# Performance work log

Hardware: AMD Instinct MI355X
Metric: run time of the kernel (lower is better)

Reference implementation:

```python
import jax, jax.numpy as jnp
import numpy as np

L, D, FF, H, S, B = 6, 512, 2048, 8, 1024, 4
DH = D // H
EPS = 1e-5


def setup_inputs() -> dict:
    key = jax.random.key(0)
    ks = jax.random.split(key, 8)
    sd = 1.0 / np.sqrt(D)
    sf = 1.0 / np.sqrt(FF)
    return {
        'src': jax.random.normal(ks[0], (S, B, D), jnp.float32),
        'pos': jax.random.normal(ks[1], (S, B, D), jnp.float32) * 0.02,
        'Wq': jax.random.normal(ks[2], (L, D, D), jnp.float32) * sd,
        'bq': jnp.zeros((L, D), jnp.float32),
        'Wk': jax.random.normal(ks[3], (L, D, D), jnp.float32) * sd,
        'bk': jnp.zeros((L, D), jnp.float32),
        'Wv': jax.random.normal(ks[4], (L, D, D), jnp.float32) * sd,
        'bv': jnp.zeros((L, D), jnp.float32),
        'W1': jax.random.normal(ks[5], (L, D, FF), jnp.float32) * sd,
        'b1': jnp.zeros((L, FF), jnp.float32),
        'W2': jax.random.normal(ks[6], (L, FF, D), jnp.float32) * sf,
        'b2': jnp.zeros((L, D), jnp.float32),
        'ln1_g': jnp.ones((L, D), jnp.float32),
        'ln1_b': jnp.zeros((L, D), jnp.float32),
        'ln2_g': jnp.ones((L, D), jnp.float32),
        'ln2_b': jnp.zeros((L, D), jnp.float32),
        'lnf_g': jnp.ones((D,), jnp.float32),
        'lnf_b': jnp.zeros((D,), jnp.float32),
    }


def _layernorm(x, g, b):
    m = jnp.mean(x, axis=-1, keepdims=True)
    v = jnp.mean(jnp.square(x - m), axis=-1, keepdims=True)
    return (x - m) * jax.lax.rsqrt(v + EPS) * g + b


def _encoder(src, pos, Wq, bq, Wk, bk, Wv, bv, W1, b1, W2, b2,
             ln1_g, ln1_b, ln2_g, ln2_b, lnf_g, lnf_b):
    # src, pos: (S, B, D). Each layer internally transposes to (B, S, D) and the
    # encoder transposes back; equivalently work in (B, S, D) throughout the loop.
    x = (src + pos).transpose(1, 0, 2)  # (B, S, D)
    scale = 1.0 / np.sqrt(DH)
    for i in range(L):
        # --- self-attention block (pre-norm) ---
        x1 = _layernorm(x, ln1_g[i], ln1_b[i])
        q = (x1 @ Wq[i] + bq[i]).reshape(B, S, H, DH)
        k = (x1 @ Wk[i] + bk[i]).reshape(B, S, H, DH)
        v = (x1 @ Wv[i] + bv[i]).reshape(B, S, H, DH)
        scores = jnp.einsum('bqhd,bkhd->bhqk', q, k) * scale  # (B, H, S, S)
        probs = jax.nn.softmax(scores, axis=-1)
        ctx = jnp.einsum('bhqk,bkhd->bqhd', probs, v).reshape(B, S, D)
        x = x + ctx  # dropout=0.0 -> identity
        # --- feed-forward block (pre-norm) ---
        x2 = _layernorm(x, ln2_g[i], ln2_b[i])
        h = jax.nn.relu(x2 @ W1[i] + b1[i])
        x = x + (h @ W2[i] + b2[i])
    out = x.transpose(1, 0, 2)  # back to (S, B, D)
    return _layernorm(out, lnf_g, lnf_b)


def reference(src, pos, Wq, bq, Wk, bk, Wv, bv, W1, b1, W2, b2,
              ln1_g, ln1_b, ln2_g, ln2_b, lnf_g, lnf_b):
    return _encoder(src, pos, Wq, bq, Wk, bk, Wv, bv, W1, b1, W2, b2,
                    ln1_g, ln1_b, ln2_g, ln2_b, lnf_g, lnf_b)
```

## Files before the change

### kernel.cpp

```cpp
#include <hip/hip_runtime.h>

#define L_LAYERS 6
#define DMODEL 512
#define FFDIM 2048
#define NHEAD 8
#define SEQ 1024
#define BATCH 4
#define DHEAD 64
#define MROWS (BATCH*SEQ)

typedef __attribute__((ext_vector_type(4))) float f32x4;
typedef __attribute__((ext_vector_type(8))) unsigned short u16x8;
typedef __attribute__((ext_vector_type(8))) __bf16 bf16x8;

#define DEV static __device__ __forceinline__

DEV unsigned short f32_to_bf16(float f) {
  unsigned int u = __float_as_uint(f);
  u += 0x7fffu + ((u >> 16) & 1u);
  return (unsigned short)(u >> 16);
}
DEV float bf16_to_f32(unsigned short h) {
  return __uint_as_float(((unsigned int)h) << 16);
}
DEV f32x4 mfma_bf16(u16x8 a, u16x8 b, f32x4 c) {
  return __builtin_amdgcn_mfma_f32_16x16x32_bf16(
      __builtin_bit_cast(bf16x8, a), __builtin_bit_cast(bf16x8, b), c, 0, 0, 0);
}
DEV void gload16(const unsigned short* g, unsigned short* l) {
  __builtin_amdgcn_global_load_lds(
      (const __attribute__((address_space(1))) unsigned int*)g,
      (__attribute__((address_space(3))) unsigned int*)l, 16, 0, 0);
}

__global__ __launch_bounds__(256) void k_transpose(const float* __restrict__ Win,
                                                   unsigned short* __restrict__ Wout,
                                                   int K, int N) {
  __shared__ float t[32][33];
  Win  += (size_t)blockIdx.z * K * N;
  Wout += (size_t)blockIdx.z * K * N;
  int n0 = blockIdx.x * 32, k0 = blockIdx.y * 32;
  int lx = threadIdx.x & 31, ly = threadIdx.x >> 5;
  #pragma unroll
  for (int r = 0; r < 32; r += 8)
    t[ly + r][lx] = Win[(size_t)(k0 + ly + r) * N + n0 + lx];
  __syncthreads();
  #pragma unroll
  for (int r = 0; r < 32; r += 8)
    Wout[(size_t)(n0 + ly + r) * K + k0 + lx] = f32_to_bf16(t[lx][ly + r]);
}

__global__ __launch_bounds__(256) void k_addpos_ln(const float* __restrict__ src,
                                                   const float* __restrict__ pos,
                                                   const float* __restrict__ g,
                                                   const float* __restrict__ be,
                                                   float* __restrict__ x,
                                                   unsigned short* __restrict__ o) {
  int lane = threadIdx.x & 63, wv = threadIdx.x >> 6;
  int row = blockIdx.x * 4 + wv;
  int b = row >> 10, ss = row & (SEQ-1);
  const float* sr = src + (size_t)(ss*BATCH + b) * DMODEL + lane * 8;
  const float* pr = pos + (size_t)(ss*BATCH + b) * DMODEL + lane * 8;
  f32x4 v0 = *(const f32x4*)sr + *(const f32x4*)pr;
  f32x4 v1 = *(const f32x4*)(sr + 4) + *(const f32x4*)(pr + 4);
  float* xr = x + (size_t)row * DMODEL + lane * 8;
  *(f32x4*)xr = v0;
  *(f32x4*)(xr + 4) = v1;
  float s  = v0.x+v0.y+v0.z+v0.w + v1.x+v1.y+v1.z+v1.w;
  float s2 = v0.x*v0.x+v0.y*v0.y+v0.z*v0.z+v0.w*v0.w
           + v1.x*v1.x+v1.y*v1.y+v1.z*v1.z+v1.w*v1.w;
  #pragma unroll
  for (int off = 1; off < 64; off <<= 1) { s += __shfl_xor(s, off); s2 += __shfl_xor(s2, off); }
  float mean = s * (1.0f/DMODEL);
  float var  = s2 * (1.0f/DMODEL) - mean*mean;
  float rs = rsqrtf(var + 1e-5f);
  const float* gp = g + lane*8; const float* bp = be + lane*8;
  f32x4 g0 = *(const f32x4*)gp, g1 = *(const f32x4*)(gp+4);
  f32x4 b0 = *(const f32x4*)bp, b1v = *(const f32x4*)(bp+4);
  u16x8 r;
  r[0] = f32_to_bf16((v0.x-mean)*rs*g0.x + b0.x);
  r[1] = f32_to_bf16((v0.y-mean)*rs*g0.y + b0.y);
  r[2] = f32_to_bf16((v0.z-mean)*rs*g0.z + b0.z);
  r[3] = f32_to_bf16((v0.w-mean)*rs*g0.w + b0.w);
  r[4] = f32_to_bf16((v1.x-mean)*rs*g1.x + b1v.x);
  r[5] = f32_to_bf16((v1.y-mean)*rs*g1.y + b1v.y);
  r[6] = f32_to_bf16((v1.z-mean)*rs*g1.z + b1v.z);
  r[7] = f32_to_bf16((v1.w-mean)*rs*g1.w + b1v.w);
  *(u16x8*)(o + (size_t)row * DMODEL + lane * 8) = r;
}

__global__ __launch_bounds__(256) void k_ln_bf16(const float* __restrict__ x,
                                                 const float* __restrict__ g,
                                                 const float* __restrict__ be,
                                                 unsigned short* __restrict__ o) {
  int lane = threadIdx.x & 63, wv = threadIdx.x >> 6;
  int row = blockIdx.x * 4 + wv;
  const float* xr = x + (size_t)row * DMODEL + lane * 8;
  f32x4 v0 = *(const f32x4*)xr, v1 = *(const f32x4*)(xr + 4);
  float s  = v0.x+v0.y+v0.z+v0.w + v1.x+v1.y+v1.z+v1.w;
  float s2 = v0.x*v0.x+v0.y*v0.y+v0.z*v0.z+v0.w*v0.w
           + v1.x*v1.x+v1.y*v1.y+v1.z*v1.z+v1.w*v1.w;
  #pragma unroll
  for (int off = 1; off < 64; off <<= 1) { s += __shfl_xor(s, off); s2 += __shfl_xor(s2, off); }
  float mean = s * (1.0f/DMODEL);
  float var  = s2 * (1.0f/DMODEL) - mean*mean;
  float rs = rsqrtf(var + 1e-5f);
  const float* gp = g + lane*8; const float* bp = be + lane*8;
  f32x4 g0 = *(const f32x4*)gp, g1 = *(const f32x4*)(gp+4);
  f32x4 b0 = *(const f32x4*)bp, b1v = *(const f32x4*)(bp+4);
  u16x8 r;
  r[0] = f32_to_bf16((v0.x-mean)*rs*g0.x + b0.x);
  r[1] = f32_to_bf16((v0.y-mean)*rs*g0.y + b0.y);
  r[2] = f32_to_bf16((v0.z-mean)*rs*g0.z + b0.z);
  r[3] = f32_to_bf16((v0.w-mean)*rs*g0.w + b0.w);
  r[4] = f32_to_bf16((v1.x-mean)*rs*g1.x + b1v.x);
  r[5] = f32_to_bf16((v1.y-mean)*rs*g1.y + b1v.y);
  r[6] = f32_to_bf16((v1.z-mean)*rs*g1.z + b1v.z);
  r[7] = f32_to_bf16((v1.w-mean)*rs*g1.w + b1v.w);
  *(u16x8*)(o + (size_t)row * DMODEL + lane * 8) = r;
}

__global__ __launch_bounds__(256) void k_ln_final(const float* __restrict__ x,
                                                  const float* __restrict__ g,
                                                  const float* __restrict__ be,
                                                  float* __restrict__ out) {
  int lane = threadIdx.x & 63, wv = threadIdx.x >> 6;
  int row = blockIdx.x * 4 + wv;
  const float* xr = x + (size_t)row * DMODEL + lane * 8;
  f32x4 v0 = *(const f32x4*)xr, v1 = *(const f32x4*)(xr + 4);
  float s  = v0.x+v0.y+v0.z+v0.w + v1.x+v1.y+v1.z+v1.w;
  float s2 = v0.x*v0.x+v0.y*v0.y+v0.z*v0.z+v0.w*v0.w
           + v1.x*v1.x+v1.y*v1.y+v1.z*v1.z+v1.w*v1.w;
  #pragma unroll
  for (int off = 1; off < 64; off <<= 1) { s += __shfl_xor(s, off); s2 += __shfl_xor(s2, off); }
  float mean = s * (1.0f/DMODEL);
  float var  = s2 * (1.0f/DMODEL) - mean*mean;
  float rs = rsqrtf(var + 1e-5f);
  const float* gp = g + lane*8; const float* bp = be + lane*8;
  f32x4 g0 = *(const f32x4*)gp, g1 = *(const f32x4*)(gp+4);
  f32x4 b0 = *(const f32x4*)bp, b1v = *(const f32x4*)(bp+4);
  int b = row >> 10, ss = row & (SEQ-1);
  float* orow = out + (size_t)(ss*BATCH + b) * DMODEL + lane * 8;
  f32x4 o0, o1;
  o0.x = (v0.x-mean)*rs*g0.x + b0.x;  o0.y = (v0.y-mean)*rs*g0.y + b0.y;
  o0.z = (v0.z-mean)*rs*g0.z + b0.z;  o0.w = (v0.w-mean)*rs*g0.w + b0.w;
  o1.x = (v1.x-mean)*rs*g1.x + b1v.x; o1.y = (v1.y-mean)*rs*g1.y + b1v.y;
  o1.z = (v1.z-mean)*rs*g1.z + b1v.z; o1.w = (v1.w-mean)*rs*g1.w + b1v.w;
  *(f32x4*)orow = o0;
  *(f32x4*)(orow + 4) = o1;
}

#define BM 128
#define BN 128
#define BKK 32
#define NSL 4

DEV void gemm_core(const unsigned short* __restrict__ A,
                   const unsigned short* __restrict__ Bt,
                   int K, int m0, int n0,
                   unsigned short* As, unsigned short* Bs, f32x4 acc[4][4]) {
  const int tid = threadIdx.x;
  const int lane = tid & 63;
  const int w = tid >> 6;
  const int wr = w >> 1, wc = w & 1;
  const int l15 = lane & 15;
  const int ko = (lane >> 4) * 8;
  const int rl = lane >> 2;
  const int cc = (lane & 3) * 8;
  for (int kb = 0; kb < K; kb += NSL * BKK) {
    #pragma unroll
    for (int sl = 0; sl < NSL; ++sl) {
      #pragma unroll
      for (int i = 0; i < 2; ++i) {
        int r0 = w * 32 + i * 16;
        gload16(A  + (size_t)(m0 + r0 + rl) * K + kb + sl * BKK + cc, As + sl * (BM*BKK) + r0 * BKK);
        gload16(Bt + (size_t)(n0 + r0 + rl) * K + kb + sl * BKK + cc, Bs + sl * (BN*BKK) + r0 * BKK);
      }
    }
    __syncthreads();
    #pragma unroll
    for (int sl = 0; sl < NSL; ++sl) {
      const unsigned short* Asl = As + sl * (BM*BKK);
      const unsigned short* Bsl = Bs + sl * (BN*BKK);
      u16x8 af[4], bfr[4];
      #pragma unroll
      for (int m = 0; m < 4; ++m) af[m]  = *(const u16x8*)(Asl + (wr*64 + m*16 + l15) * BKK + ko);
      #pragma unroll
      for (int n = 0; n < 4; ++n) bfr[n] = *(const u16x8*)(Bsl + (wc*64 + n*16 + l15) * BKK + ko);
      #pragma unroll
      for (int m = 0; m < 4; ++m)
        #pragma unroll
        for (int n = 0; n < 4; ++n)
          acc[m][n] = mfma_bf16(af[m], bfr[n], acc[m][n]);
    }
    __syncthreads();
  }
}

__global__ __launch_bounds__(256) void k_gemm_qkv(
    const unsigned short* __restrict__ x1,
    const unsigned short* __restrict__ WqT, const unsigned short* __restrict__ WkT,
    const unsigned short* __restrict__ WvT,
    const float* __restrict__ bq, const float* __restrict__ bk, const float* __restrict__ bv,
    unsigned short* __restrict__ qo, unsigned short* __restrict__ ko2,
    unsigned short* __restrict__ vo) {
  __shared__ __align__(16) unsigned short As[NSL*BM*BKK];
  __shared__ __align__(16) unsigned short Bs[NSL*64*BKK];
  const int tid = threadIdx.x;
  const int lane = tid & 63;
  const int w = tid >> 6;
  const int wr = w >> 1, wc = w & 1;
  const int l15 = lane & 15;
  const int ko = (lane >> 4) * 8;
  const int rl = lane >> 2;
  const int cc = (lane & 3) * 8;
  const int m0 = blockIdx.x * BM;
  const int mat = blockIdx.y >> 3;
  const int n0 = (blockIdx.y & 7) * 64;
  const unsigned short* Bt = (mat == 0) ? WqT : ((mat == 1) ? WkT : WvT);
  const float* bias        = (mat == 0) ? bq  : ((mat == 1) ? bk  : bv);
  unsigned short* out      = (mat == 0) ? qo  : ((mat == 1) ? ko2 : vo);
  const float osc = (mat == 0) ? 0.125f : 1.0f;
  f32x4 acc[4][2];
  #pragma unroll
  for (int m = 0; m < 4; ++m)
    #pragma unroll
    for (int n = 0; n < 2; ++n) acc[m][n] = 0.0f;
  for (int kb = 0; kb < DMODEL; kb += NSL * BKK) {
    #pragma unroll
    for (int sl = 0; sl < NSL; ++sl) {
      #pragma unroll
      for (int i = 0; i < 2; ++i) {
        int r0 = w * 32 + i * 16;
        gload16(x1 + (size_t)(m0 + r0 + rl) * DMODEL + kb + sl * BKK + cc, As + sl * (BM*BKK) + r0 * BKK);
      }
      {
        int r0 = w * 16;
        gload16(Bt + (size_t)(n0 + r0 + rl) * DMODEL + kb + sl * BKK + cc, Bs + sl * (64*BKK) + r0 * BKK);
      }
    }
    __syncthreads();
    #pragma unroll
    for (int sl = 0; sl < NSL; ++sl) {
      const unsigned short* Asl = As + sl * (BM*BKK);
      const unsigned short* Bsl = Bs + sl * (64*BKK);
      u16x8 af[4], bfr[2];
      #pragma unroll
      for (int m = 0; m < 4; ++m) af[m]  = *(const u16x8*)(Asl + (wr*64 + m*16 + l15) * BKK + ko);
      #pragma unroll
      for (int n = 0; n < 2; ++n) bfr[n] = *(const u16x8*)(Bsl + (wc*32 + n*16 + l15) * BKK + ko);
      #pragma unroll
      for (int m = 0; m < 4; ++m)
        #pragma unroll
        for (int n = 0; n < 2; ++n)
          acc[m][n] = mfma_bf16(af[m], bfr[n], acc[m][n]);
    }
    __syncthreads();
  }
  const int g = lane >> 4;
  #pragma unroll
  for (int m = 0; m < 4; ++m) {
    #pragma unroll
    for (int n = 0; n < 2; ++n) {
      int col = n0 + wc*32 + n*16 + l15;
      int hh = col >> 6, dh = col & 63;
      float bval = bias[col];
      #pragma unroll
      for (int i = 0; i < 4; ++i) {
        int row = m0 + wr*64 + m*16 + g*4 + i;
        int bb = row >> 10, ss = row & (SEQ-1);
        size_t oidx;
        if (mat == 2)
          oidx = ((((size_t)(bb*NHEAD + hh)) * DHEAD + dh) << 10) + ss;
        else
          oidx = ((((size_t)(bb*NHEAD + hh)) << 10) + ss) * DHEAD + dh;
        out[oidx] = f32_to_bf16((acc[m][n][i] + bval) * osc);
      }
    }
  }
}

__global__ __launch_bounds__(256) void k_gemm_ffn1(
    const unsigned short* __restrict__ x1, const unsigned short* __restrict__ W1T,
    const float* __restrict__ b1, unsigned short* __restrict__ h) {
  __shared__ __align__(16) unsigned short As[NSL*BM*BKK];
  __shared__ __align__(16) unsigned short Bs[NSL*BN*BKK];
  int m0 = blockIdx.x * BM, n0 = blockIdx.y * BN;
  f32x4 acc[4][4];
  #pragma unroll
  for (int m = 0; m < 4; ++m)
    #pragma unroll
    for (int n = 0; n < 4; ++n) acc[m][n] = 0.0f;
  gemm_core(x1, W1T, DMODEL, m0, n0, As, Bs, acc);
  const int lane = threadIdx.x & 63;
  const int w = threadIdx.x >> 6; const int wr = w >> 1, wc = w & 1;
  #pragma unroll
  for (int m = 0; m < 4; ++m) {
    #pragma unroll
    for (int n = 0; n < 4; ++n) {
      int col = n0 + wc*64 + n*16 + (lane & 15);
      float bval = b1[col];
      #pragma unroll
      for (int i = 0; i < 4; ++i) {
        int row = m0 + wr*64 + m*16 + (lane >> 4)*4 + i;
        h[(size_t)row * FFDIM + col] = f32_to_bf16(fmaxf(acc[m][n][i] + bval, 0.0f));
      }
    }
  }
}

#define NSL2 8
__global__ __launch_bounds__(256) void k_gemm_ffn2(
    const unsigned short* __restrict__ h, const unsigned short* __restrict__ W2T,
    const float* __restrict__ b2, float* __restrict__ x) {
  __shared__ __align__(16) unsigned short As[NSL2*64*BKK];
  __shared__ __align__(16) unsigned short Bs[NSL2*64*BKK];
  const int tid = threadIdx.x;
  const int lane = tid & 63;
  const int w = tid >> 6;
  const int wr = w >> 1, wc = w & 1;
  const int l15 = lane & 15;
  const int ko = (lane >> 4) * 8;
  const int rl = lane >> 2;
  const int cc = (lane & 3) * 8;
  const int m0 = blockIdx.x * 64, n0 = blockIdx.y * 64;
  f32x4 acc[2][2];
  #pragma unroll
  for (int m = 0; m < 2; ++m)
    #pragma unroll
    for (int n = 0; n < 2; ++n) acc[m][n] = 0.0f;
  for (int kb = 0; kb < FFDIM; kb += NSL2 * BKK) {
    #pragma unroll
    for (int sl = 0; sl < NSL2; ++sl) {
      int r0 = w * 16;
      gload16(h   + (size_t)(m0 + r0 + rl) * FFDIM + kb + sl * BKK + cc, As + sl * (64*BKK) + r0 * BKK);
      gload16(W2T + (size_t)(n0 + r0 + rl) * FFDIM + kb + sl * BKK + cc, Bs + sl * (64*BKK) + r0 * BKK);
    }
    __syncthreads();
    #pragma unroll
    for (int sl = 0; sl < NSL2; ++sl) {
      const unsigned short* Asl = As + sl * (64*BKK);
      const unsigned short* Bsl = Bs + sl * (64*BKK);
      u16x8 af[2], bfr[2];
      #pragma unroll
      for (int m = 0; m < 2; ++m) af[m]  = *(const u16x8*)(Asl + (wr*32 + m*16 + l15) * BKK + ko);
      #pragma unroll
      for (int n = 0; n < 2; ++n) bfr[n] = *(const u16x8*)(Bsl + (wc*32 + n*16 + l15) * BKK + ko);
      #pragma unroll
      for (int m = 0; m < 2; ++m)
        #pragma unroll
        for (int n = 0; n < 2; ++n)
          acc[m][n] = mfma_bf16(af[m], bfr[n], acc[m][n]);
    }
    __syncthreads();
  }
  const int g = lane >> 4;
  #pragma unroll
  for (int m = 0; m < 2; ++m) {
    #pragma unroll
    for (int n = 0; n < 2; ++n) {
      int col = n0 + wc*32 + n*16 + l15;
      float bval = b2[col];
      #pragma unroll
      for (int i = 0; i < 4; ++i) {
        int row = m0 + wr*32 + m*16 + g*4 + i;
        size_t idx = (size_t)row * DMODEL + col;
        x[idx] = x[idx] + acc[m][n][i] + bval;
      }
    }
  }
}

#define KVBLK 128
#define KP 72
#define VP 136
#define NT (SEQ/KVBLK)

__global__ __launch_bounds__(512) void k_attn_mfma(
    const unsigned short* __restrict__ qb,
    const unsigned short* __restrict__ kb,
    const unsigned short* __restrict__ vtb,
    float* __restrict__ x) {
  __shared__ __align__(16) unsigned short Kl[2][KVBLK*KP];
  __shared__ __align__(16) unsigned short Vl[2][DHEAD*VP];
  __shared__ __align__(16) unsigned short Pl[8*16*VP];
  const int tid = threadIdx.x;
  const int w = tid >> 6, lane = tid & 63;
  const int c = lane & 15, g = lane >> 4;
  const int bh = blockIdx.x, qt = blockIdx.y;
  const int qw = qt * 128 + w * 16;
  const int krow = tid >> 2, kcol = (tid & 3) * 16;
  const int vrow = tid >> 3, vcol = (tid & 7) * 16;

  const unsigned short* kbase = kb + (size_t)bh * SEQ * DHEAD;
  const unsigned short* vbase = vtb + (size_t)bh * DHEAD * SEQ;

  u16x8 qf[2];
  {
    const unsigned short* qrow = qb + ((size_t)bh * SEQ + qw + c) * DHEAD;
    qf[0] = *(const u16x8*)(qrow + g * 8);
    qf[1] = *(const u16x8*)(qrow + 32 + g * 8);
  }
  f32x4 aco[4];
  #pragma unroll
  for (int n = 0; n < 4; ++n) aco[n] = 0.0f;
  float l_r = 0.0f;

  u16x8 kr0, kr1, vr0, vr1;
  kr0 = *(const u16x8*)(kbase + (size_t)krow * DHEAD + kcol);
  kr1 = *(const u16x8*)(kbase + (size_t)krow * DHEAD + kcol + 8);
  vr0 = *(const u16x8*)(vbase + (size_t)vrow * SEQ + vcol);
  vr1 = *(const u16x8*)(vbase + (size_t)vrow * SEQ + vcol + 8);
  *(u16x8*)(Kl[0] + krow * KP + kcol)     = kr0;
  *(u16x8*)(Kl[0] + krow * KP + kcol + 8) = kr1;
  *(u16x8*)(Vl[0] + vrow * VP + vcol)     = vr0;
  *(u16x8*)(Vl[0] + vrow * VP + vcol + 8) = vr1;
  __syncthreads();

  int cur = 0;
  for (int t = 0; t < NT; ++t) {
    if (t < NT - 1) {
      int kn = (t + 1) * KVBLK;
      kr0 = *(const u16x8*)(kbase + (size_t)(kn + krow) * DHEAD + kcol);
      kr1 = *(const u16x8*)(kbase + (size_t)(kn + krow) * DHEAD + kcol + 8);
      vr0 = *(const u16x8*)(vbase + (size_t)vrow * SEQ + kn + vcol);
      vr1 = *(const u16x8*)(vbase + (size_t)vrow * SEQ + kn + vcol + 8);
    }
    const unsigned short* Kt = Kl[cur];
    const unsigned short* Vt = Vl[cur];

    f32x4 s[8];
    #pragma unroll
    for (int n = 0; n < 8; ++n) s[n] = 0.0f;
    #pragma unroll
    for (int n = 0; n < 8; ++n) {
      #pragma unroll
      for (int kk = 0; kk < 2; ++kk) {
        u16x8 kf = *(const u16x8*)(Kt + (n * 16 + c) * KP + kk * 32 + g * 8);
        s[n] = mfma_bf16(kf, qf[kk], s[n]);
      }
    }

    float ps = 0.0f;
    {
      unsigned short* prow = Pl + (w * 16 + c) * VP;
      #pragma unroll
      for (int n = 0; n < 8; ++n) {
        float p0 = __expf(s[n][0]), p1 = __expf(s[n][1]);
        float p2 = __expf(s[n][2]), p3 = __expf(s[n][3]);
        ps += (p0 + p1) + (p2 + p3);
        *(unsigned int*)(prow + n * 16 + g * 4) =
            (unsigned)f32_to_bf16(p0) | ((unsigned)f32_to_bf16(p1) << 16);
        *(unsigned int*)(prow + n * 16 + g * 4 + 2) =
            (unsigned)f32_to_bf16(p2) | ((unsigned)f32_to_bf16(p3) << 16);
      }
    }
    ps += __shfl_xor(ps, 16);
    ps += __shfl_xor(ps, 32);
    l_r += ps;

    u16x8 pa[4];
    #pragma unroll
    for (int kk = 0; kk < 4; ++kk)
      pa[kk] = *(const u16x8*)(Pl + (w * 16 + c) * VP + kk * 32 + g * 8);
    #pragma unroll
    for (int n = 0; n < 4; ++n) {
      #pragma unroll
      for (int kk = 0; kk < 4; ++kk) {
        u16x8 vf = *(const u16x8*)(Vt + (n * 16 + c) * VP + kk * 32 + g * 8);
        aco[n] = mfma_bf16(pa[kk], vf, aco[n]);
      }
    }

    if (t < NT - 1) {
      unsigned short* Kn = Kl[cur ^ 1];
      unsigned short* Vn = Vl[cur ^ 1];
      *(u16x8*)(Kn + krow * KP + kcol)     = kr0;
      *(u16x8*)(Kn + krow * KP + kcol + 8) = kr1;
      *(u16x8*)(Vn + vrow * VP + vcol)     = vr0;
      *(u16x8*)(Vn + vrow * VP + vcol + 8) = vr1;
      __syncthreads();
    }
    cur ^= 1;
  }

  const int b = bh >> 3, h = bh & 7;
  #pragma unroll
  for (int i = 0; i < 4; ++i) {
    float lq = __shfl(l_r, g * 4 + i);
    float inv = 1.0f / lq;
    int q = qw + g * 4 + i;
    float* xr = x + ((size_t)b * SEQ + q) * DMODEL + h * DHEAD;
    #pragma unroll
    for (int n = 0; n < 4; ++n)
      xr[n * 16 + c] += aco[n][i] * inv;
  }
}

extern "C" void kernel_launch(void* const* d_in, const int* in_sizes, int n_in,
                              void* d_out, int out_size, void* d_ws, size_t ws_size,
                              hipStream_t stream) {
  const float* src  = (const float*)d_in[0];
  const float* pos  = (const float*)d_in[1];
  const float* Wq   = (const float*)d_in[2];
  const float* bq   = (const float*)d_in[3];
  const float* Wk   = (const float*)d_in[4];
  const float* bk   = (const float*)d_in[5];
  const float* Wv   = (const float*)d_in[6];
  const float* bv   = (const float*)d_in[7];
  const float* W1   = (const float*)d_in[8];
  const float* b1   = (const float*)d_in[9];
  const float* W2   = (const float*)d_in[10];
  const float* b2   = (const float*)d_in[11];
  const float* ln1g = (const float*)d_in[12];
  const float* ln1b = (const float*)d_in[13];
  const float* ln2g = (const float*)d_in[14];
  const float* ln2b = (const float*)d_in[15];
  const float* lnfg = (const float*)d_in[16];
  const float* lnfb = (const float*)d_in[17];

  char* p = (char*)d_ws;
  float* x = (float*)p;                      p += (size_t)MROWS * DMODEL * 4;
  unsigned short* x1 = (unsigned short*)p;   p += (size_t)MROWS * DMODEL * 2;
  unsigned short* qb = (unsigned short*)p;   p += (size_t)MROWS * DMODEL * 2;
  unsigned short* kbuf = (unsigned short*)p; p += (size_t)MROWS * DMODEL * 2;
  unsigned short* vtbuf = (unsigned short*)p; p += (size_t)MROWS * DMODEL * 2;
  unsigned short* hbuf = (unsigned short*)p; p += (size_t)MROWS * FFDIM * 2;
  unsigned short* WqT = (unsigned short*)p;  p += (size_t)L_LAYERS * DMODEL * DMODEL * 2;
  unsigned short* WkT = (unsigned short*)p;  p += (size_t)L_LAYERS * DMODEL * DMODEL * 2;
  unsigned short* WvT = (unsigned short*)p;  p += (size_t)L_LAYERS * DMODEL * DMODEL * 2;
  unsigned short* W1T = (unsigned short*)p;  p += (size_t)L_LAYERS * DMODEL * FFDIM * 2;
  unsigned short* W2T = (unsigned short*)p;  p += (size_t)L_LAYERS * DMODEL * FFDIM * 2;

  k_transpose<<<dim3(16,16,6), 256, 0, stream>>>(Wq, WqT, DMODEL, DMODEL);
  k_transpose<<<dim3(16,16,6), 256, 0, stream>>>(Wk, WkT, DMODEL, DMODEL);
  k_transpose<<<dim3(16,16,6), 256, 0, stream>>>(Wv, WvT, DMODEL, DMODEL);
  k_transpose<<<dim3(64,16,6), 256, 0, stream>>>(W1, W1T, DMODEL, FFDIM);
  k_transpose<<<dim3(16,64,6), 256, 0, stream>>>(W2, W2T, FFDIM, DMODEL);

  for (int l = 0; l < L_LAYERS; ++l) {
    if (l == 0)
      k_addpos_ln<<<1024, 256, 0, stream>>>(src, pos, ln1g, ln1b, x, x1);
    else
      k_ln_bf16<<<1024, 256, 0, stream>>>(x, ln1g + l*DMODEL, ln1b + l*DMODEL, x1);
    k_gemm_qkv<<<dim3(32,24), 256, 0, stream>>>(
        x1,
        WqT + (size_t)l*DMODEL*DMODEL, WkT + (size_t)l*DMODEL*DMODEL, WvT + (size_t)l*DMODEL*DMODEL,
        bq + l*DMODEL, bk + l*DMODEL, bv + l*DMODEL,
        qb, kbuf, vtbuf);
    k_attn_mfma<<<dim3(32,8), 512, 0, stream>>>(qb, kbuf, vtbuf, x);
    k_ln_bf16<<<1024, 256, 0, stream>>>(x, ln2g + l*DMODEL, ln2b + l*DMODEL, x1);
    k_gemm_ffn1<<<dim3(32,16), 256, 0, stream>>>(x1, W1T + (size_t)l*DMODEL*FFDIM, b1 + l*FFDIM, hbuf);
    k_gemm_ffn2<<<dim3(64,8), 256, 0, stream>>>(hbuf, W2T + (size_t)l*DMODEL*FFDIM, b2 + l*DMODEL, x);
  }
  k_ln_final<<<1024, 256, 0, stream>>>(x, lnfg, lnfb, (float*)d_out);
}
```

Baseline: 487.3 us.

## Load attention K fragments directly into registers, bypassing shared memory

The attention kernel no longer stages K tiles in LDS. Each lane loads its MFMA K fragments straight from global memory into two register arrays that are double-buffered by unrolling the loop two tiles at a time. V stays in LDS. The launch bounds now request 2 blocks per CU. This removes the LDS write and read traffic for K and halves the LDS footprint. In exchange it raises register pressure (32 u16x8 values per lane) and replaces coalesced K loads with strided 16-byte per-lane global loads.

```diff
diff --git a/kernel.cpp b/kernel.cpp
--- a/kernel.cpp
+++ b/kernel.cpp
@@ -372,16 +372,14 @@
 }
 
 #define KVBLK 128
-#define KP 72
 #define VP 136
 #define NT (SEQ/KVBLK)
 
-__global__ __launch_bounds__(512) void k_attn_mfma(
+__global__ __launch_bounds__(512, 2) void k_attn_mfma(
     const unsigned short* __restrict__ qb,
     const unsigned short* __restrict__ kb,
     const unsigned short* __restrict__ vtb,
     float* __restrict__ x) {
-  __shared__ __align__(16) unsigned short Kl[2][KVBLK*KP];
   __shared__ __align__(16) unsigned short Vl[2][DHEAD*VP];
   __shared__ __align__(16) unsigned short Pl[8*16*VP];
   const int tid = threadIdx.x;
@@ -389,7 +387,6 @@
   const int c = lane & 15, g = lane >> 4;
   const int bh = blockIdx.x, qt = blockIdx.y;
   const int qw = qt * 128 + w * 16;
-  const int krow = tid >> 2, kcol = (tid & 3) * 16;
   const int vrow = tid >> 3, vcol = (tid & 7) * 16;
 
   const unsigned short* kbase = kb + (size_t)bh * SEQ * DHEAD;
@@ -406,83 +403,85 @@
   for (int n = 0; n < 4; ++n) aco[n] = 0.0f;
   float l_r = 0.0f;
 
-  u16x8 kr0, kr1, vr0, vr1;
-  kr0 = *(const u16x8*)(kbase + (size_t)krow * DHEAD + kcol);
-  kr1 = *(const u16x8*)(kbase + (size_t)krow * DHEAD + kcol + 8);
+  u16x8 kf0[16], kf1[16];
+  u16x8 vr0, vr1;
+
+  #pragma unroll
+  for (int n = 0; n < 8; ++n) {
+    kf0[n*2 + 0] = *(const u16x8*)(kbase + (size_t)(n*16 + c) * DHEAD + g * 8);
+    kf0[n*2 + 1] = *(const u16x8*)(kbase + (size_t)(n*16 + c) * DHEAD + 32 + g * 8);
+  }
   vr0 = *(const u16x8*)(vbase + (size_t)vrow * SEQ + vcol);
   vr1 = *(const u16x8*)(vbase + (size_t)vrow * SEQ + vcol + 8);
-  *(u16x8*)(Kl[0] + krow * KP + kcol)     = kr0;
-  *(u16x8*)(Kl[0] + krow * KP + kcol + 8) = kr1;
   *(u16x8*)(Vl[0] + vrow * VP + vcol)     = vr0;
   *(u16x8*)(Vl[0] + vrow * VP + vcol + 8) = vr1;
   __syncthreads();
 
-  int cur = 0;
-  for (int t = 0; t < NT; ++t) {
-    if (t < NT - 1) {
-      int kn = (t + 1) * KVBLK;
-      kr0 = *(const u16x8*)(kbase + (size_t)(kn + krow) * DHEAD + kcol);
-      kr1 = *(const u16x8*)(kbase + (size_t)(kn + krow) * DHEAD + kcol + 8);
-      vr0 = *(const u16x8*)(vbase + (size_t)vrow * SEQ + kn + vcol);
-      vr1 = *(const u16x8*)(vbase + (size_t)vrow * SEQ + kn + vcol + 8);
-    }
-    const unsigned short* Kt = Kl[cur];
-    const unsigned short* Vt = Vl[cur];
-
-    f32x4 s[8];
-    #pragma unroll
-    for (int n = 0; n < 8; ++n) s[n] = 0.0f;
-    #pragma unroll
-    for (int n = 0; n < 8; ++n) {
-      #pragma unroll
-      for (int kk = 0; kk < 2; ++kk) {
-        u16x8 kf = *(const u16x8*)(Kt + (n * 16 + c) * KP + kk * 32 + g * 8);
-        s[n] = mfma_bf16(kf, qf[kk], s[n]);
-      }
-    }
-
-    float ps = 0.0f;
-    {
-      unsigned short* prow = Pl + (w * 16 + c) * VP;
-      #pragma unroll
-      for (int n = 0; n < 8; ++n) {
-        float p0 = __expf(s[n][0]), p1 = __expf(s[n][1]);
-        float p2 = __expf(s[n][2]), p3 = __expf(s[n][3]);
-        ps += (p0 + p1) + (p2 + p3);
-        *(unsigned int*)(prow + n * 16 + g * 4) =
-            (unsigned)f32_to_bf16(p0) | ((unsigned)f32_to_bf16(p1) << 16);
-        *(unsigned int*)(prow + n * 16 + g * 4 + 2) =
-            (unsigned)f32_to_bf16(p2) | ((unsigned)f32_to_bf16(p3) << 16);
-      }
-    }
-    ps += __shfl_xor(ps, 16);
-    ps += __shfl_xor(ps, 32);
-    l_r += ps;
-
-    u16x8 pa[4];
-    #pragma unroll
-    for (int kk = 0; kk < 4; ++kk)
-      pa[kk] = *(const u16x8*)(Pl + (w * 16 + c) * VP + kk * 32 + g * 8);
-    #pragma unroll
-    for (int n = 0; n < 4; ++n) {
-      #pragma unroll
-      for (int kk = 0; kk < 4; ++kk) {
-        u16x8 vf = *(const u16x8*)(Vt + (n * 16 + c) * VP + kk * 32 + g * 8);
-        aco[n] = mfma_bf16(pa[kk], vf, aco[n]);
-      }
-    }
-
-    if (t < NT - 1) {
-      unsigned short* Kn = Kl[cur ^ 1];
-      unsigned short* Vn = Vl[cur ^ 1];
-      *(u16x8*)(Kn + krow * KP + kcol)     = kr0;
-      *(u16x8*)(Kn + krow * KP + kcol + 8) = kr1;
-      *(u16x8*)(Vn + vrow * VP + vcol)     = vr0;
-      *(u16x8*)(Vn + vrow * VP + vcol + 8) = vr1;
-      __syncthreads();
-    }
-    cur ^= 1;
-  }
+#define ATT_TILE(KFC, KFN, T)                                                     \
+  {                                                                               \
+    const int t_ = (T);                                                           \
+    if (t_ < NT - 1) {                                                            \
+      const int kn_ = (t_ + 1) * KVBLK;                                           \
+      const unsigned short* kt_ = kbase + (size_t)kn_ * DHEAD;                    \
+      _Pragma("unroll")                                                           \
+      for (int n = 0; n < 8; ++n) {                                               \
+        KFN[n*2 + 0] = *(const u16x8*)(kt_ + (size_t)(n*16 + c) * DHEAD + g * 8);      \
+        KFN[n*2 + 1] = *(const u16x8*)(kt_ + (size_t)(n*16 + c) * DHEAD + 32 + g * 8); \
+      }                                                                           \
+      vr0 = *(const u16x8*)(vbase + (size_t)vrow * SEQ + kn_ + vcol);             \
+      vr1 = *(const u16x8*)(vbase + (size_t)vrow * SEQ + kn_ + vcol + 8);         \
+    }                                                                             \
+    const unsigned short* Vt_ = Vl[t_ & 1];                                       \
+    f32x4 s[8];                                                                   \
+    _Pragma("unroll")                                                             \
+    for (int n = 0; n < 8; ++n) s[n] = 0.0f;                                      \
+    _Pragma("unroll")                                                             \
+    for (int n = 0; n < 8; ++n) {                                                 \
+      s[n] = mfma_bf16(KFC[n*2 + 0], qf[0], s[n]);                                \
+      s[n] = mfma_bf16(KFC[n*2 + 1], qf[1], s[n]);                                \
+    }                                                                             \
+    float ps = 0.0f;                                                              \
+    {                                                                             \
+      unsigned short* prow = Pl + (w * 16 + c) * VP;                              \
+      _Pragma("unroll")                                                           \
+      for (int n = 0; n < 8; ++n) {                                               \
+        float p0 = __expf(s[n][0]), p1 = __expf(s[n][1]);                         \
+        float p2 = __expf(s[n][2]), p3 = __expf(s[n][3]);                         \
+        ps += (p0 + p1) + (p2 + p3);                                              \
+        *(unsigned int*)(prow + n * 16 + g * 4) =                                 \
+            (unsigned)f32_to_bf16(p0) | ((unsigned)f32_to_bf16(p1) << 16);        \
+        *(unsigned int*)(prow + n * 16 + g * 4 + 2) =                             \
+            (unsigned)f32_to_bf16(p2) | ((unsigned)f32_to_bf16(p3) << 16);        \
+      }                                                                           \
+    }                                                                             \
+    ps += __shfl_xor(ps, 16);                                                     \
+    ps += __shfl_xor(ps, 32);                                                     \
+    l_r += ps;                                                                    \
+    u16x8 pa[4];                                                                  \
+    _Pragma("unroll")                                                             \
+    for (int kk = 0; kk < 4; ++kk)                                                \
+      pa[kk] = *(const u16x8*)(Pl + (w * 16 + c) * VP + kk * 32 + g * 8);         \
+    _Pragma("unroll")                                                             \
+    for (int n = 0; n < 4; ++n) {                                                 \
+      _Pragma("unroll")                                                           \
+      for (int kk = 0; kk < 4; ++kk) {                                            \
+        u16x8 vf = *(const u16x8*)(Vt_ + (n * 16 + c) * VP + kk * 32 + g * 8);    \
+        aco[n] = mfma_bf16(pa[kk], vf, aco[n]);                                   \
+      }                                                                           \
+    }                                                                             \
+    if (t_ < NT - 1) {                                                            \
+      unsigned short* Vn_ = Vl[(t_ & 1) ^ 1];                                     \
+      *(u16x8*)(Vn_ + vrow * VP + vcol)     = vr0;                                \
+      *(u16x8*)(Vn_ + vrow * VP + vcol + 8) = vr1;                                \
+      __syncthreads();                                                            \
+    }                                                                             \
+  }
+
+  for (int tp = 0; tp < NT; tp += 2) {
+    ATT_TILE(kf0, kf1, tp);
+    ATT_TILE(kf1, kf0, tp + 1);
+  }
+#undef ATT_TILE
 
   const int b = bh >> 3, h = bh & 7;
   #pragma unroll
```

Measured after the change: 610.5 us. 1.25x slower.
